# Performance work log

Measured on AMD Instinct MI355X. Metric: run time of the kernel, lower is better.

Reference implementation:

```python
import jax, jax.numpy as jnp
import numpy as np

B_, L_, DM = 8, 1024, 256
DS, DC, EX = 16, 4, 2
DI = EX * DM            # d_inner = 512
DTR = max(1, DM // 16)  # dt_rank = 16


def setup_inputs() -> dict:
    key = jax.random.key(0)
    ks = iter(jax.random.split(key, 40))
    def n(shape, s=0.02):
        return jax.random.normal(next(ks), shape, jnp.float32) * s
    inp = {"x": jax.random.normal(next(ks), (B_, L_, DM), jnp.float32)}
    inp["norm_g"] = jnp.ones((DM,), jnp.float32)
    inp["norm_b"] = jnp.zeros((DM,), jnp.float32)
    for m in ("f", "b"):
        inp[f"inW_{m}"] = n((DM, 2 * DI))
        inp[f"convW_{m}"] = n((DI, DC))
        inp[f"convB_{m}"] = jnp.zeros((DI,), jnp.float32)
        inp[f"xW_{m}"] = n((DI, DTR + 2 * DS))
        inp[f"dtW_{m}"] = n((DTR, DI))
        inp[f"dtB_{m}"] = jnp.zeros((DI,), jnp.float32)
        # ALog init: log of [1..dState] repeated over dInner rows
        inp[f"ALog_{m}"] = jnp.log(jnp.tile(jnp.arange(1, DS + 1, dtype=jnp.float32), (DI, 1)))
        inp[f"Dp_{m}"] = jnp.ones((DI,), jnp.float32)
        inp[f"outW_{m}"] = n((DI, DM))
    inp["fusW"] = n((2 * DM, DM))
    inp["fusB"] = jnp.zeros((DM,), jnp.float32)
    return inp


def _dw_conv(x, w, b):
    # causal depthwise conv1d: x [B,L,DI], w [DI,DC] -> [B,L,DI]
    xc = jnp.transpose(x, (0, 2, 1))  # B,DI,L
    out = jax.lax.conv_general_dilated(
        xc, w[:, None, :], window_strides=(1,), padding=[(DC - 1, 0)],
        dimension_numbers=("NCH", "OIH", "NCH"), feature_group_count=DI)
    return jnp.transpose(out + b[:, None], (0, 2, 1))


def _ssm(x, xW, dtW, dtB, ALog, Dp):
    # x: [B,L,DI]
    A = -jnp.exp(ALog)                                   # [DI,DS]
    xdbl = x @ xW                                        # [B,L,DTR+2*DS]
    dlt, Bp, Cp = jnp.split(xdbl, [DTR, DTR + DS], axis=-1)
    delta = jax.nn.softplus(dlt @ dtW + dtB)             # [B,L,DI]
    dA = jnp.exp(delta[..., None] * A)                   # [B,L,DI,DS]
    dBx = (delta * x)[..., None] * Bp[:, :, None, :]     # [B,L,DI,DS]

    def step(h, t):
        a, bb, c = t
        h = a * h + bb                                   # [B,DI,DS]
        y = jnp.einsum('bdn,bn->bd', h, c)
        return h, y

    h0 = jnp.zeros((x.shape[0], DI, DS), x.dtype)
    _, ys = jax.lax.scan(step, h0, (jnp.moveaxis(dA, 1, 0),
                                    jnp.moveaxis(dBx, 1, 0),
                                    jnp.moveaxis(Cp, 1, 0)))
    return jnp.moveaxis(ys, 0, 1) + Dp * x               # [B,L,DI]


def _mamba(x, inW, convW, convB, xW, dtW, dtB, ALog, Dp, outW):
    xr = x @ inW                                         # [B,L,2*DI]
    xs, res = jnp.split(xr, 2, axis=-1)
    xs = jax.nn.silu(_dw_conv(xs, convW, convB))
    y = _ssm(xs, xW, dtW, dtB, ALog, Dp)
    return (y * jax.nn.silu(res)) @ outW                 # [B,L,DM]


def reference(x, norm_g, norm_b,
              inW_f, convW_f, convB_f, xW_f, dtW_f, dtB_f, ALog_f, Dp_f, outW_f,
              inW_b, convW_b, convB_b, xW_b, dtW_b, dtB_b, ALog_b, Dp_b, outW_b,
              fusW, fusB):
    # LayerNorm
    mu = x.mean(-1, keepdims=True)
    var = ((x - mu) ** 2).mean(-1, keepdims=True)
    xn = (x - mu) * jax.lax.rsqrt(var + 1e-5) * norm_g + norm_b
    # forward-direction Mamba
    xf = _mamba(xn, inW_f, convW_f, convB_f, xW_f, dtW_f, dtB_f, ALog_f, Dp_f, outW_f)
    # backward-direction Mamba (flip along time)
    xb = _mamba(jnp.flip(xn, 1), inW_b, convW_b, convB_b, xW_b, dtW_b, dtB_b, ALog_b, Dp_b, outW_b)
    xb = jnp.flip(xb, 1)
    fused = jnp.concatenate([xf, xb], axis=-1) @ fusW + fusB
    return x + fused  # dropout is identity in eval
```

## Files before the change

kernel.cpp:

```cpp
#include <hip/hip_runtime.h>
#include <cmath>

typedef __bf16 bf16x8 __attribute__((ext_vector_type(8)));
typedef __bf16 bf16x4 __attribute__((ext_vector_type(4)));
typedef float  f32x4  __attribute__((ext_vector_type(4)));
typedef float  f32x2  __attribute__((ext_vector_type(2)));

#define B_  8
#define L_  1024
#define DM  256
#define DI  512
#define DS  16
#define DTR 16
#define M_  (B_*L_)
#define NC  64
#define CT  16

__device__ inline float softplus_f(float z){
  return (z > 20.f) ? z : __logf(1.f + __expf(z));
}
__device__ inline float silu_f(float z){
  return z / (1.f + __expf(-z));
}

__device__ inline int flag_from_x(const void* x){
  const unsigned short* u = (const unsigned short*)x;
  int lane = threadIdx.x & 63;
  unsigned short v = u[2*lane];
  int e = (v >> 7) & 0xFF;
  unsigned long long m = __ballot(e >= 160 || e < 96);
  return __popcll(m) > 16;
}

struct PrepJob { const void* src; void* dst; int rows; int cols; int f32out; };
struct PrepArgs { PrepJob j[26]; int nj; };
struct TJob { const void* src; __bf16* dst; int R; int C; };
struct TArgs { TJob j[3]; int ntiles[3]; int nj; int ntot; };

__global__ __launch_bounds__(256) void wprep_k(TArgs ta, PrepArgs a, const void* xsrc){
  const int f = flag_from_x(xsrc);
  const int tid = threadIdx.x;
  if ((int)blockIdx.x < ta.ntot){
    __shared__ float tile[64][65];
    int bid = blockIdx.x;
    int jj = 0;
    while (jj < ta.nj-1 && bid >= ta.ntiles[jj]) { bid -= ta.ntiles[jj]; jj++; }
    const TJob J = ta.j[jj];
    const int tpr = J.C >> 6;
    const int tr = bid / tpr, tc = bid - tr*tpr;
    const int r0 = tr*64, c0 = tc*64;
    #pragma unroll
    for (int i=0;i<16;i++){
      int idx = i*256 + tid;
      int r = idx >> 6, c = idx & 63;
      long off = (long)(r0+r)*J.C + c0 + c;
      tile[r][c] = f ? ((const float*)J.src)[off] : (float)((const __bf16*)J.src)[off];
    }
    __syncthreads();
    #pragma unroll
    for (int i=0;i<16;i++){
      int idx = i*256 + tid;
      int c = idx >> 6, r = idx & 63;
      J.dst[(long)(c0+c)*J.R + r0 + r] = (__bf16)tile[r][c];
    }
  } else {
    int e = (blockIdx.x - ta.ntot)*256 + tid;
    #pragma unroll 1
    for (int jj=0; jj<a.nj; jj++){
      int sz = a.j[jj].rows * a.j[jj].cols;
      if (e < sz){
        int cols = a.j[jj].cols;
        int r = e / cols, c = e - r*cols;
        float v = f ? ((const float*)a.j[jj].src)[e] : (float)((const __bf16*)a.j[jj].src)[e];
        if (a.j[jj].f32out) ((float*)a.j[jj].dst)[c*a.j[jj].rows + r] = v;
        else ((__bf16*)a.j[jj].dst)[(long)c*a.j[jj].rows + r] = (__bf16)v;
        return;
      }
      e -= sz;
    }
  }
}

__global__ __launch_bounds__(256) void lnw_k(
    const void* x, const __bf16* g, const __bf16* bb, __bf16* xn,
    const __bf16* fusWt, const __bf16* outWr0, const __bf16* outWr1,
    __bf16* BtC0, __bf16* BtC1)
{
  const int bx = blockIdx.x;
  const int tid = threadIdx.x;
  const int lane = tid & 63;
  const int wid = tid >> 6;

  if (bx < M_/4){
    const int f = flag_from_x(x);
    long row = (long)bx*4 + wid;
    long base = row*DM + lane*4;
    float v0,v1,v2,v3;
    if (f){ f32x4 xv = *(const f32x4*)((const float*)x + base);
            v0=xv[0]; v1=xv[1]; v2=xv[2]; v3=xv[3]; }
    else  { bf16x4 xv = *(const bf16x4*)((const __bf16*)x + base);
            v0=(float)xv[0]; v1=(float)xv[1]; v2=(float)xv[2]; v3=(float)xv[3]; }
    float s = v0+v1+v2+v3;
    float q = v0*v0+v1*v1+v2*v2+v3*v3;
    #pragma unroll
    for (int off=32; off>0; off>>=1){ s += __shfl_xor(s,off); q += __shfl_xor(q,off); }
    float mu = s*(1.f/DM), var = q*(1.f/DM)-mu*mu;
    float rs = rsqrtf(var+1e-5f);
    bf16x4 gv = *(const bf16x4*)(g + lane*4);
    bf16x4 bv = *(const bf16x4*)(bb + lane*4);
    bf16x4 o;
    o[0]=(__bf16)((v0-mu)*rs*(float)gv[0]+(float)bv[0]);
    o[1]=(__bf16)((v1-mu)*rs*(float)gv[1]+(float)bv[1]);
    o[2]=(__bf16)((v2-mu)*rs*(float)gv[2]+(float)bv[2]);
    o[3]=(__bf16)((v3-mu)*rs*(float)gv[3]+(float)bv[3]);
    *(bf16x4*)(xn + base) = o;
  } else {
    int b2 = bx - M_/4;
    int wz  = b2 >> 5;
    int rem = b2 & 31;
    int gx = rem & 3, gy = rem >> 2;
    const __bf16* A  = fusWt + wz*DM;
    const __bf16* Bt = wz ? outWr1 : outWr0;
    __bf16* C = wz ? BtC1 : BtC0;
    const int mBase = (gx*4 + wid)*16;
    const int nBase = gy*64;
    const int lm = lane & 15;
    const int kq = (lane >> 4)*8;
    long aoff = (long)(mBase+lm)*(2*DM) + kq;
    long boff[4];
    #pragma unroll
    for (int j=0;j<4;j++) boff[j] = (long)(nBase+j*16+lm)*DM + kq;
    f32x4 acc[4] = {};
    #pragma unroll
    for (int k0=0;k0<DM;k0+=32){
      bf16x8 af = *(const bf16x8*)(A + aoff + k0);
      bf16x8 bfr[4];
      #pragma unroll
      for (int j=0;j<4;j++) bfr[j] = *(const bf16x8*)(Bt + boff[j] + k0);
      #pragma unroll
      for (int j=0;j<4;j++)
        acc[j] = __builtin_amdgcn_mfma_f32_16x16x32_bf16(af, bfr[j], acc[j], 0,0,0);
    }
    #pragma unroll
    for (int rr=0;rr<4;rr++){
      int r = mBase + (lane>>4)*4 + rr;
      #pragma unroll
      for (int j=0;j<4;j++){
        int c = nBase + j*16 + lm;
        C[(long)r*DI + c] = (__bf16)acc[j][rr];
      }
    }
  }
}

template<int BM,int BN,int KK>
__global__ __launch_bounds__(256) void gemm_in_k(
    const __bf16* A, const __bf16* B0, const __bf16* B1,
    __bf16* xz0, __bf16* xz1, __bf16* res0, __bf16* res1,
    int lda, int ldb)
{
  constexpr int TM = BM/2, TN = BN/2;
  constexpr int WMT = TM/16, WNT = TN/16;
  constexpr int LA = BM/64, LB = BN/64;

  const int dir = blockIdx.z;
  const __bf16* Bt = dir ? B1 : B0;
  __bf16* xz  = dir ? xz1 : xz0;
  __bf16* res = dir ? res1 : res0;
  const int tid  = threadIdx.x;
  const int lane = tid & 63;
  const int wid  = tid >> 6;
  const int wm = wid & 1;
  const int wn = wid >> 1;
  const int mBase = blockIdx.x * BM;
  const int nBase = blockIdx.y * BN;
  const int lm = lane & 15;
  const int kq = (lane >> 4) * 8;

  __shared__ __bf16 As[BM*32];
  __shared__ __bf16 Bs[BN*32];

  const __bf16* aS[LA];
  const __bf16* bS[LB];
  {
    int colk = (tid & 3) * 8;
    #pragma unroll
    for (int ld=0; ld<LA; ld++){
      int r = mBase + ld*64 + (tid >> 2);
      if (dir==1){ int b = r >> 10, t = r & (L_-1); r = (b<<10) + (L_-1-t); }
      aS[ld] = A + (long)r*lda + colk;
    }
    #pragma unroll
    for (int ld=0; ld<LB; ld++){
      int r = nBase + ld*64 + (tid >> 2);
      bS[ld] = Bt + (long)r*ldb + colk;
    }
  }

  f32x4 acc[WMT][WNT] = {};
  for (int k0=0; k0<KK; k0+=32){
    #pragma unroll
    for (int ld=0; ld<LA; ld++)
      __builtin_amdgcn_global_load_lds(
        (const __attribute__((address_space(1))) void*)(aS[ld] + k0),
        (__attribute__((address_space(3))) void*)(&As[ld*2048 + tid*8]), 16, 0, 0);
    #pragma unroll
    for (int ld=0; ld<LB; ld++)
      __builtin_amdgcn_global_load_lds(
        (const __attribute__((address_space(1))) void*)(bS[ld] + k0),
        (__attribute__((address_space(3))) void*)(&Bs[ld*2048 + tid*8]), 16, 0, 0);
    __syncthreads();
    bf16x8 af[WMT], bfr[WNT];
    #pragma unroll
    for (int i=0;i<WMT;i++) af[i]  = *(const bf16x8*)&As[(wm*TM + i*16 + lm)*32 + kq];
    #pragma unroll
    for (int j=0;j<WNT;j++) bfr[j] = *(const bf16x8*)&Bs[(wn*TN + j*16 + lm)*32 + kq];
    #pragma unroll
    for (int i=0;i<WMT;i++)
      #pragma unroll
      for (int j=0;j<WNT;j++)
        acc[i][j] = __builtin_amdgcn_mfma_f32_16x16x32_bf16(af[i], bfr[j], acc[i][j], 0,0,0);
    __syncthreads();
  }

  #pragma unroll
  for (int i=0;i<WMT;i++){
    #pragma unroll
    for (int rr=0;rr<4;rr++){
      int r = mBase + wm*TM + i*16 + (lane>>4)*4 + rr;
      #pragma unroll
      for (int j=0;j<WNT;j++){
        int c = nBase + wn*TN + j*16 + lm;
        float v = acc[i][j][rr];
        if (c < DI) xz[(long)r*DI + c] = (__bf16)v;
        else        res[(long)r*DI + (c-DI)] = (__bf16)v;
      }
    }
  }
}

template<int BM,int BN,int KK>
__global__ __launch_bounds__(256) void gemm_fin_k(
    const __bf16* Af, const __bf16* Ab,
    const __bf16* Bt0, const __bf16* Bt1,
    void* Cout, const __bf16* bias, const void* resid)
{
  constexpr int TM = BM/2, TN = BN/2;
  constexpr int WMT = TM/16, WNT = TN/16;
  constexpr int LA = BM/64, LB = BN/64;

  const int of = flag_from_x(resid);
  const int tid  = threadIdx.x;
  const int lane = tid & 63;
  const int wid  = tid >> 6;
  const int wm = wid & 1;
  const int wn = wid >> 1;
  const int mBase = blockIdx.x * BM;
  const int nBase = blockIdx.y * BN;
  const int lm = lane & 15;
  const int kq = (lane >> 4) * 8;

  __shared__ __bf16 As[BM*32];
  __shared__ __bf16 Bs[BN*32];

  f32x4 acc[WMT][WNT] = {};
  #pragma unroll 1
  for (int dd=0; dd<2; dd++){
    const __bf16* A  = dd ? Ab  : Af;
    const __bf16* Bt = dd ? Bt1 : Bt0;
    const __bf16* aS[LA];
    const __bf16* bS[LB];
    {
      int colk = (tid & 3) * 8;
      #pragma unroll
      for (int ld=0; ld<LA; ld++){
        int r = mBase + ld*64 + (tid >> 2);
        if (dd==1){ int b = r >> 10, t = r & (L_-1); r = (b<<10) + (L_-1-t); }
        aS[ld] = A + (long)r*DI + colk;
      }
      #pragma unroll
      for (int ld=0; ld<LB; ld++){
        int r = nBase + ld*64 + (tid >> 2);
        bS[ld] = Bt + (long)r*DI + colk;
      }
    }
    for (int k0=0; k0<KK; k0+=32){
      #pragma unroll
      for (int ld=0; ld<LA; ld++)
        __builtin_amdgcn_global_load_lds(
          (const __attribute__((address_space(1))) void*)(aS[ld] + k0),
          (__attribute__((address_space(3))) void*)(&As[ld*2048 + tid*8]), 16, 0, 0);
      #pragma unroll
      for (int ld=0; ld<LB; ld++)
        __builtin_amdgcn_global_load_lds(
          (const __attribute__((address_space(1))) void*)(bS[ld] + k0),
          (__attribute__((address_space(3))) void*)(&Bs[ld*2048 + tid*8]), 16, 0, 0);
      __syncthreads();
      bf16x8 af[WMT], bfr[WNT];
      #pragma unroll
      for (int i=0;i<WMT;i++) af[i]  = *(const bf16x8*)&As[(wm*TM + i*16 + lm)*32 + kq];
      #pragma unroll
      for (int j=0;j<WNT;j++) bfr[j] = *(const bf16x8*)&Bs[(wn*TN + j*16 + lm)*32 + kq];
      #pragma unroll
      for (int i=0;i<WMT;i++)
        #pragma unroll
        for (int j=0;j<WNT;j++)
          acc[i][j] = __builtin_amdgcn_mfma_f32_16x16x32_bf16(af[i], bfr[j], acc[i][j], 0,0,0);
      __syncthreads();
    }
  }

  #pragma unroll
  for (int i=0;i<WMT;i++){
    #pragma unroll
    for (int rr=0;rr<4;rr++){
      int r = mBase + wm*TM + i*16 + (lane>>4)*4 + rr;
      #pragma unroll
      for (int j=0;j<WNT;j++){
        int c = nBase + wn*TN + j*16 + lm;
        float v = acc[i][j][rr];
        float rsd = of ? ((const float*)resid)[(long)r*DM + c]
                       : (float)((const __bf16*)resid)[(long)r*DM + c];
        v += (float)bias[c] + rsd;
        if (of) ((float*)Cout)[(long)r*DM + c] = v;
        else    ((__bf16*)Cout)[(long)r*DM + c] = (__bf16)v;
      }
    }
  }
}

__global__ __launch_bounds__(512) void scanA_k(
    const __bf16* xz0, const __bf16* xz1,
    const float* cw0, const float* cw1,
    const __bf16* cb0, const __bf16* cb1,
    const __bf16* xW0, const __bf16* xW1,
    const float* dw0, const float* dw1,
    const __bf16* dtB0, const __bf16* dtB1,
    const float* ALf0, const float* ALf1,
    float* hend, float* sumd)
{
  const int dir = blockIdx.z;
  const __bf16* xz  = dir ? xz1 : xz0;
  const float*  cw  = dir ? cw1 : cw0;
  const __bf16* cb  = dir ? cb1 : cb0;
  const __bf16* xWt = dir ? xW1 : xW0;
  const float*  dw  = dir ? dw1 : dw0;
  const __bf16* dtB = dir ? dtB1 : dtB0;
  const float*  ALf = dir ? ALf1 : ALf0;

  const int b   = blockIdx.y;
  const int c   = blockIdx.x;
  const int tid = threadIdx.x;
  const int lane = tid & 63;
  const int wid  = tid >> 6;
  const int d   = tid;
  const int db  = dir*8 + b;
  const long row0 = (long)b*L_ + c*CT;

  __shared__ __bf16 xs_s[CT*DI];
  __shared__ float  sX[CT][32];

  {
    const float c0 = cw[0*DI+d], c1 = cw[1*DI+d], c2 = cw[2*DI+d], c3 = cw[3*DI+d];
    const float cbv = (float)cb[d];
    int gt0 = c*CT;
    float xm3 = (gt0-3 >= 0) ? (float)xz[(row0-3)*DI + d] : 0.f;
    float xm2 = (gt0-2 >= 0) ? (float)xz[(row0-2)*DI + d] : 0.f;
    float xm1 = (gt0-1 >= 0) ? (float)xz[(row0-1)*DI + d] : 0.f;
    #pragma unroll
    for (int t=0;t<CT;t++){
      float xt = (float)xz[(row0+t)*DI + d];
      float a = cbv;
      a += xm3*c0; a += xm2*c1; a += xm1*c2; a += xt*c3;
      float sv = silu_f(a);
      *(__bf16*)((char*)xs_s + t*1024 + ((2*d) ^ ((t&7)<<4))) = (__bf16)sv;
      xm3 = xm2; xm2 = xm1; xm1 = xt;
    }
  }
  __syncthreads();

  if (wid < 2){
    const int nb = wid * 16;
    const int lm = lane & 15;
    const int kq = (lane >> 4) * 8;
    const int row = lm;
    const char* abase = (const char*)xs_s + row*1024;
    const int rsw = (row&7)<<4;
    const __bf16* Bt = xWt + (long)(nb + lm)*DI + kq;
    f32x4 acc = {};
    #pragma unroll
    for (int k0=0;k0<DI;k0+=32){
      bf16x8 af  = *(const bf16x8*)(abase + (((kq + k0)*2) ^ rsw));
      bf16x8 bfr = *(const bf16x8*)(Bt + k0);
      acc = __builtin_amdgcn_mfma_f32_16x16x32_bf16(af, bfr, acc, 0,0,0);
    }
    #pragma unroll
    for (int rr=0;rr<4;rr++){
      int r = (lane>>4)*4 + rr;
      sX[r][nb + lm] = acc[rr];
    }
  }

  f32x2 dw2[8];
  { const f32x4* p = (const f32x4*)(dw + d*DTR);
    #pragma unroll
    for (int q=0;q<4;q++){ f32x4 v=p[q];
      dw2[q*2]   = f32x2{v[0],v[1]};
      dw2[q*2+1] = f32x2{v[2],v[3]}; } }
  bool pow_ok = true;
  #pragma unroll 1
  for (int n=0;n<16;n++){
    float An = -__expf(ALf[d*DS + n]);
    pow_ok = pow_ok && (fabsf(An + (float)(n+1)) < 0.003f*(n+1));
  }
  const float dtbv = (float)dtB[d];

  f32x2 h2[8];
  #pragma unroll
  for (int i=0;i<8;i++) h2[i] = f32x2{0.f,0.f};
  float sdelta = 0.f;
  __syncthreads();

  if (pow_ok){
    #pragma unroll 2
    for (int t=0;t<CT;t++){
      f32x2 z2 = f32x2{dtbv, 0.f};
      #pragma unroll
      for (int i=0;i<8;i++){
        f32x2 qv = *(const f32x2*)&sX[t][i*2];
        z2 += qv*dw2[i];
      }
      float delta = softplus_f(z2[0]+z2[1]);
      sdelta += delta;
      float xv = (float)*(const __bf16*)((const char*)xs_s + t*1024 + ((2*d) ^ ((t&7)<<4)));
      float dx = delta*xv;
      f32x2 dx2 = f32x2{dx, dx};
      float e1 = __expf(-delta), e2v = e1*e1;
      f32x2 e22 = f32x2{e2v, e2v};
      f32x2 pw = f32x2{e1, e2v};
      #pragma unroll
      for (int i=0;i<8;i++){
        f32x2 Bv = *(const f32x2*)&sX[t][16+i*2];
        h2[i] = pw*h2[i] + dx2*Bv;
        pw = pw*e22;
      }
    }
  } else {
    #pragma unroll 2
    for (int t=0;t<CT;t++){
      f32x2 z2 = f32x2{dtbv, 0.f};
      #pragma unroll
      for (int i=0;i<8;i++){
        f32x2 qv = *(const f32x2*)&sX[t][i*2];
        z2 += qv*dw2[i];
      }
      float delta = softplus_f(z2[0]+z2[1]);
      sdelta += delta;
      float xv = (float)*(const __bf16*)((const char*)xs_s + t*1024 + ((2*d) ^ ((t&7)<<4)));
      float dx = delta*xv;
      #pragma unroll
      for (int i=0;i<8;i++){
        f32x2 A2 = f32x2{-__expf(ALf[d*DS+i*2]), -__expf(ALf[d*DS+i*2+1])};
        f32x2 Bv = *(const f32x2*)&sX[t][16+i*2];
        f32x2 pw = f32x2{__expf(delta*A2[0]), __expf(delta*A2[1])};
        h2[i] = pw*h2[i] + f32x2{dx,dx}*Bv;
      }
    }
  }

  long hb = (((long)db*NC + c)*DI + d)*16;
  f32x4* hp = (f32x4*)(hend + hb);
  #pragma unroll
  for (int q=0;q<4;q++){
    f32x4 v; v[0]=h2[q*2][0]; v[1]=h2[q*2][1]; v[2]=h2[q*2+1][0]; v[3]=h2[q*2+1][1];
    hp[q]=v;
  }
  sumd[((long)db*NC + c)*DI + d] = sdelta;
}

__global__ __launch_bounds__(256) void scanB_k(
    const float* ALf0, const float* ALf1,
    const float* hend, const float* sumd, float* Hbuf)
{
  int gid = blockIdx.x*256 + threadIdx.x;
  int n  = gid & 15;
  int d  = (gid>>4) & 511;
  int db = gid >> 13;
  const float* ALf = (db>=8) ? ALf1 : ALf0;
  float A_dn = -__expf(ALf[d*DS + n]);
  const long base0 = (((long)db*NC)*DI + d)*16 + n;
  const long cstr  = (long)DI*16;
  const long sbase = (long)db*NC*DI + d;
  float H = 0.f;
  #pragma unroll 1
  for (int g=0; g<NC/16; g++){
    float he[16], Sv[16];
    #pragma unroll
    for (int k=0;k<16;k++){
      he[k] = hend[base0 + (long)(g*16+k)*cstr];
      Sv[k] = sumd[sbase + (long)(g*16+k)*DI];
    }
    #pragma unroll
    for (int k=0;k<16;k++){
      Hbuf[base0 + (long)(g*16+k)*cstr] = H;
      H = he[k] + __expf(A_dn*Sv[k])*H;
    }
  }
}

__global__ __launch_bounds__(512) void scanC_k(
    const __bf16* xz0, const __bf16* xz1,
    const float* cw0, const float* cw1,
    const __bf16* cb0, const __bf16* cb1,
    const __bf16* xW0, const __bf16* xW1,
    __bf16* res0, __bf16* res1,
    const float* dw0, const float* dw1,
    const __bf16* dtB0, const __bf16* dtB1,
    const float* ALf0, const float* ALf1,
    const __bf16* Dp0, const __bf16* Dp1,
    const float* Hbuf)
{
  const int dir = blockIdx.z;
  const __bf16* xz  = dir ? xz1 : xz0;
  const float*  cw  = dir ? cw1 : cw0;
  const __bf16* cb  = dir ? cb1 : cb0;
  const __bf16* xWt = dir ? xW1 : xW0;
  __bf16*       res = dir ? res1 : res0;
  const float*  dw  = dir ? dw1 : dw0;
  const __bf16* dtB = dir ? dtB1 : dtB0;
  const float*  ALf = dir ? ALf1 : ALf0;
  const __bf16* Dp  = dir ? Dp1 : Dp0;

  const int b   = blockIdx.y;
  const int c   = blockIdx.x;
  const int tid = threadIdx.x;
  const int lane = tid & 63;
  const int wid  = tid >> 6;
  const int d   = tid;
  const int db  = dir*8 + b;
  const long row0 = (long)b*L_ + c*CT;

  __shared__ __bf16 xs_s[CT*DI];
  __shared__ float  sX[CT][48];

  {
    const float c0 = cw[0*DI+d], c1 = cw[1*DI+d], c2 = cw[2*DI+d], c3 = cw[3*DI+d];
    const float cbv = (float)cb[d];
    int gt0 = c*CT;
    float xm3 = (gt0-3 >= 0) ? (float)xz[(row0-3)*DI + d] : 0.f;
    float xm2 = (gt0-2 >= 0) ? (float)xz[(row0-2)*DI + d] : 0.f;
    float xm1 = (gt0-1 >= 0) ? (float)xz[(row0-1)*DI + d] : 0.f;
    #pragma unroll
    for (int t=0;t<CT;t++){
      float xt = (float)xz[(row0+t)*DI + d];
      float a = cbv;
      a += xm3*c0; a += xm2*c1; a += xm1*c2; a += xt*c3;
      float sv = silu_f(a);
      *(__bf16*)((char*)xs_s + t*1024 + ((2*d) ^ ((t&7)<<4))) = (__bf16)sv;
      xm3 = xm2; xm2 = xm1; xm1 = xt;
    }
  }
  __syncthreads();

  if (wid < 3){
    const int nb = wid * 16;
    const int lm = lane & 15;
    const int kq = (lane >> 4) * 8;
    const int row = lm;
    const char* abase = (const char*)xs_s + row*1024;
    const int rsw = (row&7)<<4;
    const __bf16* Bt = xWt + (long)(nb + lm)*DI + kq;
    f32x4 acc = {};
    #pragma unroll
    for (int k0=0;k0<DI;k0+=32){
      bf16x8 af  = *(const bf16x8*)(abase + (((kq + k0)*2) ^ rsw));
      bf16x8 bfr = *(const bf16x8*)(Bt + k0);
      acc = __builtin_amdgcn_mfma_f32_16x16x32_bf16(af, bfr, acc, 0,0,0);
    }
    #pragma unroll
    for (int rr=0;rr<4;rr++){
      int r = (lane>>4)*4 + rr;
      sX[r][nb + lm] = acc[rr];
    }
  }

  f32x2 dw2[8];
  { const f32x4* p = (const f32x4*)(dw + d*DTR);
    #pragma unroll
    for (int q=0;q<4;q++){ f32x4 v=p[q];
      dw2[q*2]   = f32x2{v[0],v[1]};
      dw2[q*2+1] = f32x2{v[2],v[3]}; } }
  bool pow_ok = true;
  #pragma unroll 1
  for (int n=0;n<16;n++){
    float An = -__expf(ALf[d*DS + n]);
    pow_ok = pow_ok && (fabsf(An + (float)(n+1)) < 0.003f*(n+1));
  }
  const float dtbv = (float)dtB[d];

  f32x2 h2[8];
  { long hb = (((long)db*NC + c)*DI + d)*16;
    const f32x4* p = (const f32x4*)(Hbuf + hb);
    #pragma unroll
    for (int q=0;q<4;q++){ f32x4 v = p[q];
      h2[q*2]   = f32x2{v[0],v[1]};
      h2[q*2+1] = f32x2{v[2],v[3]}; } }
  const float Dpv = (float)Dp[d];
  __syncthreads();

  if (pow_ok){
    #pragma unroll 2
    for (int t=0;t<CT;t++){
      long row = row0 + t;
      f32x2 z2 = f32x2{dtbv, 0.f};
      #pragma unroll
      for (int i=0;i<8;i++){
        f32x2 qv = *(const f32x2*)&sX[t][i*2];
        z2 += qv*dw2[i];
      }
      float delta = softplus_f(z2[0]+z2[1]);
      float xv = (float)*(const __bf16*)((const char*)xs_s + t*1024 + ((2*d) ^ ((t&7)<<4)));
      float dx = delta*xv;
      f32x2 dx2 = f32x2{dx, dx};
      float e1 = __expf(-delta), e2v = e1*e1;
      f32x2 e22 = f32x2{e2v, e2v};
      f32x2 pw = f32x2{e1, e2v};
      f32x2 p2 = f32x2{0.f, 0.f};
      #pragma unroll
      for (int i=0;i<8;i++){
        f32x2 Bv = *(const f32x2*)&sX[t][16+i*2];
        f32x2 Cv = *(const f32x2*)&sX[t][32+i*2];
        h2[i] = pw*h2[i] + dx2*Bv;
        p2 += h2[i]*Cv;
        pw = pw*e22;
      }
      float yv = p2[0] + p2[1] + Dpv*xv;
      float rv = (float)res[row*DI + d];
      res[row*DI + d] = (__bf16)(yv * silu_f(rv));
    }
  } else {
    #pragma unroll 2
    for (int t=0;t<CT;t++){
      long row = row0 + t;
      f32x2 z2 = f32x2{dtbv, 0.f};
      #pragma unroll
      for (int i=0;i<8;i++){
        f32x2 qv = *(const f32x2*)&sX[t][i*2];
        z2 += qv*dw2[i];
      }
      float delta = softplus_f(z2[0]+z2[1]);
      float xv = (float)*(const __bf16*)((const char*)xs_s + t*1024 + ((2*d) ^ ((t&7)<<4)));
      float dx = delta*xv;
      f32x2 p2 = f32x2{0.f, 0.f};
      #pragma unroll
      for (int i=0;i<8;i++){
        f32x2 A2 = f32x2{-__expf(ALf[d*DS+i*2]), -__expf(ALf[d*DS+i*2+1])};
        f32x2 Bv = *(const f32x2*)&sX[t][16+i*2];
        f32x2 Cv = *(const f32x2*)&sX[t][32+i*2];
        f32x2 pw = f32x2{__expf(delta*A2[0]), __expf(delta*A2[1])};
        h2[i] = pw*h2[i] + f32x2{dx,dx}*Bv;
        p2 += h2[i]*Cv;
      }
      float yv = p2[0] + p2[1] + Dpv*xv;
      float rv = (float)res[row*DI + d];
      res[row*DI + d] = (__bf16)(yv * silu_f(rv));
    }
  }
}

extern "C" void kernel_launch(void* const* d_in, const int* in_sizes, int n_in,
                              void* d_out, int out_size, void* d_ws, size_t ws_size,
                              hipStream_t stream)
{
  const size_t MB = 1u<<20;
  if (ws_size < 160*MB) return;

  char* w = (char*)d_ws;
  __bf16* xz[2]  = {(__bf16*)(w + 0),      (__bf16*)(w + 8*MB)};
  __bf16* res[2] = {(__bf16*)(w + 16*MB),  (__bf16*)(w + 24*MB)};
  __bf16* xn     = (__bf16*)(w + 48*MB);

  char* wp = w + 52*MB;
  auto carve = [&](size_t bytes)->void*{
    void* p = wp;
    wp += (bytes + 255) & ~(size_t)255;
    return p;
  };
  __bf16 *inWt[2], *xWt[2], *outWr[2], *BtC[2];
  float *dtWt[2], *convWt[2];
  for (int m=0;m<2;m++){
    inWt[m]   = (__bf16*)carve((size_t)(2*DI)*DM*2);
    xWt[m]    = (__bf16*)carve((size_t)48*DI*2);
    outWr[m]  = (__bf16*)carve((size_t)DI*DM*2);
    BtC[m]    = (__bf16*)carve((size_t)DM*DI*2);
    dtWt[m]   = (float*)carve((size_t)DI*DTR*4);
    convWt[m] = (float*)carve((size_t)4*DI*4);
  }
  __bf16* fusWt = (__bf16*)carve((size_t)DM*(2*DM)*2);
  float* ALf[2] = {(float*)carve((size_t)DI*DS*4), (float*)carve((size_t)DI*DS*4)};

  char* cp = w + 57*MB;
  auto carve2 = [&](size_t elems)->__bf16*{
    __bf16* p = (__bf16*)cp;
    cp += (elems*2 + 255) & ~(size_t)255;
    return p;
  };
  __bf16* ngc = carve2(DM);
  __bf16* nbc = carve2(DM);
  __bf16 *convBc[2], *dtBc[2], *Dpc[2];
  for (int m=0;m<2;m++){
    convBc[m] = carve2(DI);
    dtBc[m]   = carve2(DI);
    Dpc[m]    = carve2(DI);
  }
  __bf16* fusBc = carve2(DM);

  float* hend = (float*)(w + 90*MB);
  float* Hbuf = (float*)(w + 122*MB);
  float* sumd = (float*)(w + 154*MB);

  PrepArgs pa;
  int ji = 0;
  size_t tot = 0;
  auto addj = [&](const void* s, void* dst, int rows, int cols, int f32o){
    pa.j[ji++] = {s, dst, rows, cols, f32o};
    tot += (size_t)rows*cols;
  };
  for (int m=0;m<2;m++){
    int base = 3 + m*9;
    addj(d_in[base+3], xWt[m],   DI,  48,   0);
    addj(d_in[base+8], outWr[m], 1,   DI*DM,0);
    addj(d_in[base+4], dtWt[m],  DTR, DI,   1);
    addj(d_in[base+1], convWt[m],DI,  4,    1);
    addj(d_in[base+2], convBc[m],1, DI, 0);
    addj(d_in[base+5], dtBc[m],  1, DI, 0);
    addj(d_in[base+6], (void*)ALf[m], 1, DI*DS, 1);
    addj(d_in[base+7], Dpc[m],   1, DI, 0);
  }
  addj(d_in[1],  ngc, 1, DM, 0);
  addj(d_in[2],  nbc, 1, DM, 0);
  addj(d_in[22], fusBc, 1, DM, 0);
  pa.nj = ji;

  TArgs ta;
  ta.j[0] = { d_in[3],  inWt[0], DM,   2*DI }; ta.ntiles[0] = (DM/64)*((2*DI)/64);
  ta.j[1] = { d_in[12], inWt[1], DM,   2*DI }; ta.ntiles[1] = (DM/64)*((2*DI)/64);
  ta.j[2] = { d_in[21], fusWt,   2*DM, DM   }; ta.ntiles[2] = ((2*DM)/64)*(DM/64);
  ta.nj = 3;
  ta.ntot = ta.ntiles[0]+ta.ntiles[1]+ta.ntiles[2];
  int prepBlocks = (int)((tot+255)/256);
  wprep_k<<<ta.ntot + prepBlocks, 256, 0, stream>>>(ta, pa, d_in[0]);

  lnw_k<<<M_/4 + 64, 256, 0, stream>>>(
      d_in[0], ngc, nbc, xn, fusWt, outWr[0], outWr[1], BtC[0], BtC[1]);

  gemm_in_k<128,128,256><<<dim3(M_/128, (2*DI)/128, 2), 256, 0, stream>>>(
      xn, inWt[0], inWt[1], xz[0], xz[1], res[0], res[1], DM, DM);

  scanA_k<<<dim3(NC, B_, 2), 512, 0, stream>>>(
      xz[0], xz[1], convWt[0], convWt[1], convBc[0], convBc[1],
      xWt[0], xWt[1], dtWt[0], dtWt[1],
      dtBc[0], dtBc[1], ALf[0], ALf[1], hend, sumd);
  scanB_k<<<131072/256, 256, 0, stream>>>(ALf[0], ALf[1], hend, sumd, Hbuf);
  scanC_k<<<dim3(NC, B_, 2), 512, 0, stream>>>(
      xz[0], xz[1], convWt[0], convWt[1], convBc[0], convBc[1],
      xWt[0], xWt[1], res[0], res[1],
      dtWt[0], dtWt[1], dtBc[0], dtBc[1], ALf[0], ALf[1], Dpc[0], Dpc[1], Hbuf);

  gemm_fin_k<64,64,DI><<<dim3(M_/64, DM/64, 1), 256, 0, stream>>>(
      res[0], res[1], BtC[0], BtC[1], d_out, fusBc, d_in[0]);
}
```

Before: 266.2 us.

## Materialize conv+x_proj outputs in scanA and consume them in scanC

scanA now processes 32-step chunks. It computes the full 48-column x_proj (delta, B and C) with six waves instead of two, and writes the SiLU-conv activations and the projections to global buffers. It also emits chunk-end states at 16 and 32 steps so that scanB still produces per-16-step starting states. scanC no longer recomputes the convolution or the MFMA projection and only reads the stored values. This removes the duplicated conv and GEMM work at the cost of extra global writes and reads, and it halves the scanA grid, which lowers parallelism in that kernel.

Result: slower. 273.2 us (+2.6%).

```diff
diff --git a/kernel.cpp b/kernel.cpp
--- a/kernel.cpp
+++ b/kernel.cpp
@@ -13,8 +13,10 @@
 #define DS  16
 #define DTR 16
 #define M_  (B_*L_)
-#define NC  64
-#define CT  16
+#define NC  32
+#define CT  32
+#define CC  64
+#define CTC 16
 
 __device__ inline float softplus_f(float z){
   return (z > 20.f) ? z : __logf(1.f + __expf(z));
@@ -337,7 +339,9 @@
     const float* dw0, const float* dw1,
     const __bf16* dtB0, const __bf16* dtB1,
     const float* ALf0, const float* ALf1,
-    float* hend, float* sumd)
+    __bf16* xg0, __bf16* xg1,
+    float* sg0, float* sg1,
+    float* hend16, float* hend32, float* sumd16, float* sumd32)
 {
   const int dir = blockIdx.z;
   const __bf16* xz  = dir ? xz1 : xz0;
@@ -347,6 +351,8 @@
   const float*  dw  = dir ? dw1 : dw0;
   const __bf16* dtB = dir ? dtB1 : dtB0;
   const float*  ALf = dir ? ALf1 : ALf0;
+  __bf16*       xg  = dir ? xg1 : xg0;
+  float*        sg  = dir ? sg1 : sg0;
 
   const int b   = blockIdx.y;
   const int c   = blockIdx.x;
@@ -355,35 +361,37 @@
   const int wid  = tid >> 6;
   const int d   = tid;
   const int db  = dir*8 + b;
-  const long row0 = (long)b*L_ + c*CT;
+  const long row0 = (long)b*L_ + (long)c*CT;
 
   __shared__ __bf16 xs_s[CT*DI];
-  __shared__ float  sX[CT][32];
+  __shared__ float  sX[CT][48];
 
   {
-    const float c0 = cw[0*DI+d], c1 = cw[1*DI+d], c2 = cw[2*DI+d], c3 = cw[3*DI+d];
+    const float q0 = cw[0*DI+d], q1 = cw[1*DI+d], q2 = cw[2*DI+d], q3 = cw[3*DI+d];
     const float cbv = (float)cb[d];
     int gt0 = c*CT;
     float xm3 = (gt0-3 >= 0) ? (float)xz[(row0-3)*DI + d] : 0.f;
     float xm2 = (gt0-2 >= 0) ? (float)xz[(row0-2)*DI + d] : 0.f;
     float xm1 = (gt0-1 >= 0) ? (float)xz[(row0-1)*DI + d] : 0.f;
-    #pragma unroll
+    #pragma unroll 8
     for (int t=0;t<CT;t++){
       float xt = (float)xz[(row0+t)*DI + d];
       float a = cbv;
-      a += xm3*c0; a += xm2*c1; a += xm1*c2; a += xt*c3;
-      float sv = silu_f(a);
-      *(__bf16*)((char*)xs_s + t*1024 + ((2*d) ^ ((t&7)<<4))) = (__bf16)sv;
+      a += xm3*q0; a += xm2*q1; a += xm1*q2; a += xt*q3;
+      __bf16 sv = (__bf16)silu_f(a);
+      *(__bf16*)((char*)xs_s + t*1024 + ((2*d) ^ ((t&7)<<4))) = sv;
+      xg[(row0+t)*DI + d] = sv;
       xm3 = xm2; xm2 = xm1; xm1 = xt;
     }
   }
   __syncthreads();
 
-  if (wid < 2){
-    const int nb = wid * 16;
+  if (wid < 6){
+    const int mb = (wid & 1) * 16;
+    const int nb = (wid >> 1) * 16;
     const int lm = lane & 15;
     const int kq = (lane >> 4) * 8;
-    const int row = lm;
+    const int row = mb + lm;
     const char* abase = (const char*)xs_s + row*1024;
     const int rsw = (row&7)<<4;
     const __bf16* Bt = xWt + (long)(nb + lm)*DI + kq;
@@ -396,8 +404,9 @@
     }
     #pragma unroll
     for (int rr=0;rr<4;rr++){
-      int r = (lane>>4)*4 + rr;
+      int r = mb + (lane>>4)*4 + rr;
       sX[r][nb + lm] = acc[rr];
+      sg[(row0 + r)*48 + nb + lm] = acc[rr];
     }
   }
 
@@ -421,66 +430,75 @@
   float sdelta = 0.f;
   __syncthreads();
 
-  if (pow_ok){
-    #pragma unroll 2
-    for (int t=0;t<CT;t++){
-      f32x2 z2 = f32x2{dtbv, 0.f};
-      #pragma unroll
-      for (int i=0;i<8;i++){
-        f32x2 qv = *(const f32x2*)&sX[t][i*2];
-        z2 += qv*dw2[i];
-      }
-      float delta = softplus_f(z2[0]+z2[1]);
-      sdelta += delta;
-      float xv = (float)*(const __bf16*)((const char*)xs_s + t*1024 + ((2*d) ^ ((t&7)<<4)));
-      float dx = delta*xv;
-      f32x2 dx2 = f32x2{dx, dx};
-      float e1 = __expf(-delta), e2v = e1*e1;
-      f32x2 e22 = f32x2{e2v, e2v};
-      f32x2 pw = f32x2{e1, e2v};
-      #pragma unroll
-      for (int i=0;i<8;i++){
-        f32x2 Bv = *(const f32x2*)&sX[t][16+i*2];
-        h2[i] = pw*h2[i] + dx2*Bv;
-        pw = pw*e22;
-      }
-    }
-  } else {
-    #pragma unroll 2
-    for (int t=0;t<CT;t++){
-      f32x2 z2 = f32x2{dtbv, 0.f};
-      #pragma unroll
-      for (int i=0;i<8;i++){
-        f32x2 qv = *(const f32x2*)&sX[t][i*2];
-        z2 += qv*dw2[i];
-      }
-      float delta = softplus_f(z2[0]+z2[1]);
-      sdelta += delta;
-      float xv = (float)*(const __bf16*)((const char*)xs_s + t*1024 + ((2*d) ^ ((t&7)<<4)));
-      float dx = delta*xv;
-      #pragma unroll
-      for (int i=0;i<8;i++){
-        f32x2 A2 = f32x2{-__expf(ALf[d*DS+i*2]), -__expf(ALf[d*DS+i*2+1])};
-        f32x2 Bv = *(const f32x2*)&sX[t][16+i*2];
-        f32x2 pw = f32x2{__expf(delta*A2[0]), __expf(delta*A2[1])};
-        h2[i] = pw*h2[i] + f32x2{dx,dx}*Bv;
-      }
-    }
-  }
-
-  long hb = (((long)db*NC + c)*DI + d)*16;
-  f32x4* hp = (f32x4*)(hend + hb);
-  #pragma unroll
-  for (int q=0;q<4;q++){
-    f32x4 v; v[0]=h2[q*2][0]; v[1]=h2[q*2][1]; v[2]=h2[q*2+1][0]; v[3]=h2[q*2+1][1];
-    hp[q]=v;
-  }
-  sumd[((long)db*NC + c)*DI + d] = sdelta;
+  auto scan16 = [&](int t0){
+    if (pow_ok){
+      #pragma unroll 2
+      for (int t=t0;t<t0+16;t++){
+        f32x2 z2 = f32x2{dtbv, 0.f};
+        #pragma unroll
+        for (int i=0;i<8;i++){
+          f32x2 qv = *(const f32x2*)&sX[t][i*2];
+          z2 += qv*dw2[i];
+        }
+        float delta = softplus_f(z2[0]+z2[1]);
+        sdelta += delta;
+        float xv = (float)*(const __bf16*)((const char*)xs_s + t*1024 + ((2*d) ^ ((t&7)<<4)));
+        float dx = delta*xv;
+        f32x2 dx2 = f32x2{dx, dx};
+        float e1 = __expf(-delta), e2v = e1*e1;
+        f32x2 e22 = f32x2{e2v, e2v};
+        f32x2 pw = f32x2{e1, e2v};
+        #pragma unroll
+        for (int i=0;i<8;i++){
+          f32x2 Bv = *(const f32x2*)&sX[t][16+i*2];
+          h2[i] = pw*h2[i] + dx2*Bv;
+          pw = pw*e22;
+        }
+      }
+    } else {
+      #pragma unroll 2
+      for (int t=t0;t<t0+16;t++){
+        f32x2 z2 = f32x2{dtbv, 0.f};
+        #pragma unroll
+        for (int i=0;i<8;i++){
+          f32x2 qv = *(const f32x2*)&sX[t][i*2];
+          z2 += qv*dw2[i];
+        }
+        float delta = softplus_f(z2[0]+z2[1]);
+        sdelta += delta;
+        float xv = (float)*(const __bf16*)((const char*)xs_s + t*1024 + ((2*d) ^ ((t&7)<<4)));
+        float dx = delta*xv;
+        #pragma unroll
+        for (int i=0;i<8;i++){
+          f32x2 A2 = f32x2{-__expf(ALf[d*DS+i*2]), -__expf(ALf[d*DS+i*2+1])};
+          f32x2 Bv = *(const f32x2*)&sX[t][16+i*2];
+          f32x2 pw = f32x2{__expf(delta*A2[0]), __expf(delta*A2[1])};
+          h2[i] = pw*h2[i] + f32x2{dx,dx}*Bv;
+        }
+      }
+    }
+  };
+  auto dump = [&](float* hd, float* sd){
+    long hb = (((long)db*NC + c)*DI + d)*16;
+    f32x4* hp = (f32x4*)(hd + hb);
+    #pragma unroll
+    for (int q=0;q<4;q++){
+      f32x4 v; v[0]=h2[q*2][0]; v[1]=h2[q*2][1]; v[2]=h2[q*2+1][0]; v[3]=h2[q*2+1][1];
+      hp[q]=v;
+    }
+    sd[((long)db*NC + c)*DI + d] = sdelta;
+  };
+
+  scan16(0);
+  dump(hend16, sumd16);
+  scan16(16);
+  dump(hend32, sumd32);
 }
 
 __global__ __launch_bounds__(256) void scanB_k(
     const float* ALf0, const float* ALf1,
-    const float* hend, const float* sumd, float* Hbuf)
+    const float* hend16, const float* hend32,
+    const float* sumd16, const float* sumd32, float* Hbuf)
 {
   int gid = blockIdx.x*256 + threadIdx.x;
   int n  = gid & 15;
@@ -488,43 +506,45 @@
   int db = gid >> 13;
   const float* ALf = (db>=8) ? ALf1 : ALf0;
   float A_dn = -__expf(ALf[d*DS + n]);
-  const long base0 = (((long)db*NC)*DI + d)*16 + n;
   const long cstr  = (long)DI*16;
-  const long sbase = (long)db*NC*DI + d;
+  const long hb = (long)db*NC*cstr + (long)d*16 + n;
+  const long sb = (long)db*NC*DI + d;
+  const long ob = (long)db*CC*cstr + (long)d*16 + n;
   float H = 0.f;
   #pragma unroll 1
-  for (int g=0; g<NC/16; g++){
-    float he[16], Sv[16];
-    #pragma unroll
-    for (int k=0;k<16;k++){
-      he[k] = hend[base0 + (long)(g*16+k)*cstr];
-      Sv[k] = sumd[sbase + (long)(g*16+k)*DI];
-    }
-    #pragma unroll
-    for (int k=0;k<16;k++){
-      Hbuf[base0 + (long)(g*16+k)*cstr] = H;
-      H = he[k] + __expf(A_dn*Sv[k])*H;
-    }
-  }
-}
-
-__global__ __launch_bounds__(512) void scanC_k(
-    const __bf16* xz0, const __bf16* xz1,
-    const float* cw0, const float* cw1,
-    const __bf16* cb0, const __bf16* cb1,
-    const __bf16* xW0, const __bf16* xW1,
-    __bf16* res0, __bf16* res1,
-    const float* dw0, const float* dw1,
-    const __bf16* dtB0, const __bf16* dtB1,
-    const float* ALf0, const float* ALf1,
-    const __bf16* Dp0, const __bf16* Dp1,
-    const float* Hbuf)
+  for (int gq=0; gq<NC/8; gq++){
+    float h16[8], h32[8], e16[8], e32[8];
+    #pragma unroll
+    for (int k=0;k<8;k++){
+      int g = gq*8+k;
+      h16[k] = hend16[hb + (long)g*cstr];
+      h32[k] = hend32[hb + (long)g*cstr];
+      e16[k] = __expf(A_dn * sumd16[sb + (long)g*DI]);
+      e32[k] = __expf(A_dn * sumd32[sb + (long)g*DI]);
+    }
+    #pragma unroll
+    for (int k=0;k<8;k++){
+      int g = gq*8+k;
+      Hbuf[ob + (long)(2*g)*cstr]   = H;
+      Hbuf[ob + (long)(2*g+1)*cstr] = h16[k] + e16[k]*H;
+      H = h32[k] + e32[k]*H;
+    }
+  }
+}
+
+__global__ __launch_bounds__(512, 8) void scanC_k(
+    const __bf16* __restrict__ xg0, const __bf16* __restrict__ xg1,
+    const float* __restrict__ sg0, const float* __restrict__ sg1,
+    __bf16* __restrict__ res0, __bf16* __restrict__ res1,
+    const float* __restrict__ dw0, const float* __restrict__ dw1,
+    const __bf16* __restrict__ dtB0, const __bf16* __restrict__ dtB1,
+    const float* __restrict__ ALf0, const float* __restrict__ ALf1,
+    const __bf16* __restrict__ Dp0, const __bf16* __restrict__ Dp1,
+    const float* __restrict__ Hbuf)
 {
   const int dir = blockIdx.z;
-  const __bf16* xz  = dir ? xz1 : xz0;
-  const float*  cw  = dir ? cw1 : cw0;
-  const __bf16* cb  = dir ? cb1 : cb0;
-  const __bf16* xWt = dir ? xW1 : xW0;
+  const __bf16* xg  = dir ? xg1 : xg0;
+  const float*  sg  = dir ? sg1 : sg0;
   __bf16*       res = dir ? res1 : res0;
   const float*  dw  = dir ? dw1 : dw0;
   const __bf16* dtB = dir ? dtB1 : dtB0;
@@ -534,55 +554,13 @@
   const int b   = blockIdx.y;
   const int c   = blockIdx.x;
   const int tid = threadIdx.x;
-  const int lane = tid & 63;
-  const int wid  = tid >> 6;
   const int d   = tid;
   const int db  = dir*8 + b;
-  const long row0 = (long)b*L_ + c*CT;
-
-  __shared__ __bf16 xs_s[CT*DI];
-  __shared__ float  sX[CT][48];
-
-  {
-    const float c0 = cw[0*DI+d], c1 = cw[1*DI+d], c2 = cw[2*DI+d], c3 = cw[3*DI+d];
-    const float cbv = (float)cb[d];
-    int gt0 = c*CT;
-    float xm3 = (gt0-3 >= 0) ? (float)xz[(row0-3)*DI + d] : 0.f;
-    float xm2 = (gt0-2 >= 0) ? (float)xz[(row0-2)*DI + d] : 0.f;
-    float xm1 = (gt0-1 >= 0) ? (float)xz[(row0-1)*DI + d] : 0.f;
-    #pragma unroll
-    for (int t=0;t<CT;t++){
-      float xt = (float)xz[(row0+t)*DI + d];
-      float a = cbv;
-      a += xm3*c0; a += xm2*c1; a += xm1*c2; a += xt*c3;
-      float sv = silu_f(a);
-      *(__bf16*)((char*)xs_s + t*1024 + ((2*d) ^ ((t&7)<<4))) = (__bf16)sv;
-      xm3 = xm2; xm2 = xm1; xm1 = xt;
-    }
-  }
-  __syncthreads();
-
-  if (wid < 3){
-    const int nb = wid * 16;
-    const int lm = lane & 15;
-    const int kq = (lane >> 4) * 8;
-    const int row = lm;
-    const char* abase = (const char*)xs_s + row*1024;
-    const int rsw = (row&7)<<4;
-    const __bf16* Bt = xWt + (long)(nb + lm)*DI + kq;
-    f32x4 acc = {};
-    #pragma unroll
-    for (int k0=0;k0<DI;k0+=32){
-      bf16x8 af  = *(const bf16x8*)(abase + (((kq + k0)*2) ^ rsw));
-      bf16x8 bfr = *(const bf16x8*)(Bt + k0);
-      acc = __builtin_amdgcn_mfma_f32_16x16x32_bf16(af, bfr, acc, 0,0,0);
-    }
-    #pragma unroll
-    for (int rr=0;rr<4;rr++){
-      int r = (lane>>4)*4 + rr;
-      sX[r][nb + lm] = acc[rr];
-    }
-  }
+  const long row0 = (long)b*L_ + (long)c*CTC;
+
+  __shared__ float sX[CTC][48];
+  if (tid < (CTC*48)/4)
+    ((f32x4*)sX)[tid] = ((const f32x4*)(sg + row0*48))[tid];
 
   f32x2 dw2[8];
   { const f32x4* p = (const f32x4*)(dw + d*DTR);
@@ -597,20 +575,20 @@
     pow_ok = pow_ok && (fabsf(An + (float)(n+1)) < 0.003f*(n+1));
   }
   const float dtbv = (float)dtB[d];
+  const float Dpv  = (float)Dp[d];
 
   f32x2 h2[8];
-  { long hb = (((long)db*NC + c)*DI + d)*16;
+  { long hb = (((long)db*CC + c)*DI + d)*16;
     const f32x4* p = (const f32x4*)(Hbuf + hb);
     #pragma unroll
     for (int q=0;q<4;q++){ f32x4 v = p[q];
       h2[q*2]   = f32x2{v[0],v[1]};
       h2[q*2+1] = f32x2{v[2],v[3]}; } }
-  const float Dpv = (float)Dp[d];
   __syncthreads();
 
   if (pow_ok){
     #pragma unroll 2
-    for (int t=0;t<CT;t++){
+    for (int t=0;t<CTC;t++){
       long row = row0 + t;
       f32x2 z2 = f32x2{dtbv, 0.f};
       #pragma unroll
@@ -619,7 +597,7 @@
         z2 += qv*dw2[i];
       }
       float delta = softplus_f(z2[0]+z2[1]);
-      float xv = (float)*(const __bf16*)((const char*)xs_s + t*1024 + ((2*d) ^ ((t&7)<<4)));
+      float xv = (float)xg[row*DI + d];
       float dx = delta*xv;
       f32x2 dx2 = f32x2{dx, dx};
       float e1 = __expf(-delta), e2v = e1*e1;
@@ -640,7 +618,7 @@
     }
   } else {
     #pragma unroll 2
-    for (int t=0;t<CT;t++){
+    for (int t=0;t<CTC;t++){
       long row = row0 + t;
       f32x2 z2 = f32x2{dtbv, 0.f};
       #pragma unroll
@@ -649,7 +627,7 @@
         z2 += qv*dw2[i];
       }
       float delta = softplus_f(z2[0]+z2[1]);
-      float xv = (float)*(const __bf16*)((const char*)xs_s + t*1024 + ((2*d) ^ ((t&7)<<4)));
+      float xv = (float)xg[row*DI + d];
       float dx = delta*xv;
       f32x2 p2 = f32x2{0.f, 0.f};
       #pragma unroll
@@ -676,9 +654,10 @@
   if (ws_size < 160*MB) return;
 
   char* w = (char*)d_ws;
-  __bf16* xz[2]  = {(__bf16*)(w + 0),      (__bf16*)(w + 8*MB)};
-  __bf16* res[2] = {(__bf16*)(w + 16*MB),  (__bf16*)(w + 24*MB)};
-  __bf16* xn     = (__bf16*)(w + 48*MB);
+  __bf16* xz[2]   = {(__bf16*)(w + 0),      (__bf16*)(w + 8*MB)};
+  __bf16* res[2]  = {(__bf16*)(w + 16*MB),  (__bf16*)(w + 24*MB)};
+  __bf16* xs_g[2] = {(__bf16*)(w + 32*MB),  (__bf16*)(w + 40*MB)};
+  __bf16* xn      = (__bf16*)(w + 48*MB);
 
   char* wp = w + 52*MB;
   auto carve = [&](size_t bytes)->void*{
@@ -715,9 +694,12 @@
   }
   __bf16* fusBc = carve2(DM);
 
-  float* hend = (float*)(w + 90*MB);
-  float* Hbuf = (float*)(w + 122*MB);
-  float* sumd = (float*)(w + 154*MB);
+  float* sXg[2] = {(float*)(w + 58*MB), (float*)(w + 60*MB)};
+  float* hend16 = (float*)(w + 64*MB);
+  float* hend32 = (float*)(w + 80*MB);
+  float* sumd16 = (float*)(w + 96*MB);
+  float* sumd32 = (float*)(w + 97*MB);
+  float* Hbuf   = (float*)(w + 98*MB);
 
   PrepArgs pa;
   int ji = 0;
@@ -760,11 +742,13 @@
   scanA_k<<<dim3(NC, B_, 2), 512, 0, stream>>>(
       xz[0], xz[1], convWt[0], convWt[1], convBc[0], convBc[1],
       xWt[0], xWt[1], dtWt[0], dtWt[1],
-      dtBc[0], dtBc[1], ALf[0], ALf[1], hend, sumd);
-  scanB_k<<<131072/256, 256, 0, stream>>>(ALf[0], ALf[1], hend, sumd, Hbuf);
-  scanC_k<<<dim3(NC, B_, 2), 512, 0, stream>>>(
-      xz[0], xz[1], convWt[0], convWt[1], convBc[0], convBc[1],
-      xWt[0], xWt[1], res[0], res[1],
+      dtBc[0], dtBc[1], ALf[0], ALf[1],
+      xs_g[0], xs_g[1], sXg[0], sXg[1],
+      hend16, hend32, sumd16, sumd32);
+  scanB_k<<<131072/256, 256, 0, stream>>>(
+      ALf[0], ALf[1], hend16, hend32, sumd16, sumd32, Hbuf);
+  scanC_k<<<dim3(CC, B_, 2), 512, 0, stream>>>(
+      xs_g[0], xs_g[1], sXg[0], sXg[1], res[0], res[1],
       dtWt[0], dtWt[1], dtBc[0], dtBc[1], ALf[0], ALf[1], Dpc[0], Dpc[1], Hbuf);
 
   gemm_fin_k<64,64,DI><<<dim3(M_/64, DM/64, 1), 256, 0, stream>>>(
```
